# Kernel tuning notes

Measured on AMD Instinct MI355X. Metric: run time of the kernel, lower is better.

## Reference

```python
import jax, jax.numpy as jnp
import numpy as np

DIM = 768
HEADS = 12
HEAD_DIM = DIM // HEADS          # 64
DIM_HALF = HEAD_DIM // 2         # 32
SPATIAL = 3


def _rope_cos_sin(grid, voxel_size, theta):
    """grid: static tuple of ints (len SPATIAL); voxel_size: [SPATIAL] float;
    theta: [H, DIM_HALF] per-head frequency spectrum.
    Returns cos, sin of shape [H, N, DIM_HALF] where N = prod(grid)."""
    axes = [jnp.arange(g, dtype=theta.dtype) for g in grid]
    mesh = jnp.meshgrid(*axes, indexing='ij')
    coords = jnp.stack([m.reshape(-1) for m in mesh], axis=-1) * voxel_size  # [N, S] physical coords
    axis_idx = np.arange(DIM_HALF) % len(grid)        # round-robin freq->axis assignment
    pos = coords[:, axis_idx]                          # [N, DIM_HALF]
    ang = pos[None, :, :] * theta[:, None, :]          # [H, N, DIM_HALF]
    return jnp.cos(ang), jnp.sin(ang)


def _rope_apply(t, cos, sin):
    # t: [B, H, N, D]; cos/sin: [H, N, DIM_HALF] broadcast over batch
    t1, t2 = jnp.split(t, 2, axis=-1)
    return jnp.concatenate([t1 * cos - t2 * sin, t1 * sin + t2 * cos], axis=-1)


def setup_inputs() -> dict:
    key = jax.random.key(0)
    k_x, k_qkv, k_proj, k_b = jax.random.split(key, 4)
    B, N = 2, 8 * 16 * 16
    x = jax.random.normal(k_x, (B, N, DIM), dtype=jnp.float32)
    voxel_size = jnp.ones((SPATIAL,), dtype=jnp.float32)
    # nn.Linear weights are [out_features, in_features]
    w_qkv = jax.random.normal(k_qkv, (3 * DIM, DIM), dtype=jnp.float32) * (DIM ** -0.5)
    w_proj = jax.random.normal(k_proj, (DIM, DIM), dtype=jnp.float32) * (DIM ** -0.5)
    b_proj = jax.random.normal(k_b, (DIM,), dtype=jnp.float32) * 0.02
    # learnable per-head base frequencies: theta_j = 10000^{-j/dim_half}
    base = (1.0 / (10000.0 ** (np.arange(DIM_HALF, dtype=np.float32) / DIM_HALF)))
    theta = jnp.asarray(np.tile(base[None, :], (HEADS, 1)))  # [H, DIM_HALF]
    return {"x": x, "voxel_size": voxel_size, "w_qkv": w_qkv, "w_proj": w_proj,
            "b_proj": b_proj, "theta": theta, "grid_d": 8, "grid_h": 16, "grid_w": 16}


def reference(x, voxel_size, w_qkv, w_proj, b_proj, theta, grid_d, grid_h, grid_w):
    B, N, dim = x.shape
    H, D = HEADS, HEAD_DIM
    qkv = jnp.einsum('bnd,ed->bne', x, w_qkv).reshape(B, N, 3, H, D)
    qkv = jnp.transpose(qkv, (2, 0, 3, 1, 4))           # [3, B, H, N, D]
    q, k, v = qkv[0], qkv[1], qkv[2]
    cos, sin = _rope_cos_sin((grid_d, grid_h, grid_w), voxel_size, theta)
    q = _rope_apply(q, cos, sin)
    k = _rope_apply(k, cos, sin)
    scale = 1.0 / np.sqrt(D).astype(np.float32)
    attn = jax.nn.softmax(jnp.einsum('bhnd,bhmd->bhnm', q, k) * scale, axis=-1)
    out = jnp.einsum('bhnm,bhmd->bhnd', attn, v)        # [B, H, N, D]
    out = jnp.transpose(out, (0, 2, 1, 3)).reshape(B, N, dim)
    return out @ w_proj.T + b_proj
```

## Files before the change

### kernel.cpp

```cpp
#include <hip/hip_runtime.h>
#include <stdint.h>

#define DIM 768
#define NHEADS 12
#define HDIM 64
#define DHALF 32
#define NTOK 2048
#define QKVN 2304
#define LOG2E 1.44269504088896340736f

typedef unsigned short u16;
typedef unsigned int u32;
typedef __bf16 bf16x8 __attribute__((ext_vector_type(8)));
typedef short s16x8 __attribute__((ext_vector_type(8)));
typedef float f32x4 __attribute__((ext_vector_type(4)));

__device__ __forceinline__ f32x4 f4zero() { f32x4 z = {0.f, 0.f, 0.f, 0.f}; return z; }

__device__ __forceinline__ u16 f2bf(float f) {
    u32 u = __builtin_bit_cast(u32, f);
    u32 r = (u + 0x7FFFu + ((u >> 16) & 1u)) >> 16;
    return (u16)r;
}

__device__ __forceinline__ void gld_lds16(void* lds, const void* g) {
    __builtin_amdgcn_global_load_lds((const __attribute__((address_space(1))) u32*)g,
                                     (__attribute__((address_space(3))) u32*)lds,
                                     16, 0, 0);
}

__global__ __launch_bounds__(256) void cast3_f32_to_bf16(const float* __restrict__ a, u16* __restrict__ oa, int na4,
                                                         const float* __restrict__ b, u16* __restrict__ ob, int nb4,
                                                         const float* __restrict__ c, u16* __restrict__ oc, int nc4) {
    int i = blockIdx.x * 256 + threadIdx.x;
    const float* src;
    u16* dst;
    int j = i;
    if (i < na4) { src = a; dst = oa; }
    else if (i < na4 + nb4) { src = b; dst = ob; j = i - na4; }
    else if (i < na4 + nb4 + nc4) { src = c; dst = oc; j = i - na4 - nb4; }
    else return;
    float4 v = ((const float4*)src)[j];
    u32 w0 = (u32)f2bf(v.x) | ((u32)f2bf(v.y) << 16);
    u32 w1 = (u32)f2bf(v.z) | ((u32)f2bf(v.w) << 16);
    ((uint2*)dst)[j] = make_uint2(w0, w1);
}

__global__ __launch_bounds__(256) void gemm_bt(const u16* __restrict__ A, const u16* __restrict__ Bm,
                                               float* __restrict__ C, const float* __restrict__ bias,
                                               int M, int N, int K) {
    __shared__ __align__(16) u16 sA[2][64 * 32];
    __shared__ __align__(16) u16 sB[2][64 * 32];
    const int t = threadIdx.x;
    const int wave = t >> 6, lane = t & 63;
    const int quad = lane >> 4, l16 = lane & 15;
    const int bm = blockIdx.y * 64, bn = blockIdx.x * 64;
    const int wr = wave >> 1, wc = wave & 1;

    f32x4 acc[2][2];
#pragma unroll
    for (int i = 0; i < 2; i++)
#pragma unroll
        for (int j = 0; j < 2; j++) acc[i][j] = f4zero();

    auto stage = [&](int k0, int bi) {
        gld_lds16((char*)&sA[bi][0] + wave * 1024,
                  A + (size_t)(bm + wave * 16 + (lane >> 2)) * K + k0 + (lane & 3) * 8);
        gld_lds16((char*)&sB[bi][0] + wave * 1024,
                  Bm + (size_t)(bn + wave * 16 + (lane >> 2)) * K + k0 + (lane & 3) * 8);
    };

    stage(0, 0);
    int cur = 0;
    for (int k0 = 0; k0 < K; k0 += 32) {
        __syncthreads();
        if (k0 + 32 < K) stage(k0 + 32, cur ^ 1);
        const u16* pA = &sA[cur][0];
        const u16* pB = &sB[cur][0];
        bf16x8 af[2], bfr[2];
#pragma unroll
        for (int mb = 0; mb < 2; mb++)
            af[mb] = *(const bf16x8*)(pA + (wr * 32 + mb * 16 + l16) * 32 + quad * 8);
#pragma unroll
        for (int nb = 0; nb < 2; nb++)
            bfr[nb] = *(const bf16x8*)(pB + (wc * 32 + nb * 16 + l16) * 32 + quad * 8);
#pragma unroll
        for (int mb = 0; mb < 2; mb++)
#pragma unroll
            for (int nb = 0; nb < 2; nb++)
                acc[mb][nb] = __builtin_amdgcn_mfma_f32_16x16x32_bf16(af[mb], bfr[nb], acc[mb][nb], 0, 0, 0);
        cur ^= 1;
    }
#pragma unroll
    for (int mb = 0; mb < 2; mb++)
#pragma unroll
        for (int nb = 0; nb < 2; nb++) {
            int col = bn + wc * 32 + nb * 16 + l16;
            float bv = bias ? bias[col] : 0.f;
#pragma unroll
            for (int r = 0; r < 4; r++) {
                int row = bm + wr * 32 + mb * 16 + quad * 4 + r;
                C[(size_t)row * N + col] = acc[mb][nb][r] + bv;
            }
        }
}

__global__ __launch_bounds__(256) void gemm_qkv_rope(const u16* __restrict__ A, const u16* __restrict__ Bm,
                                                     const float* __restrict__ voxel,
                                                     const float* __restrict__ theta,
                                                     const int* __restrict__ gh_p, const int* __restrict__ gw_p,
                                                     u16* __restrict__ q_s, u16* __restrict__ k_s,
                                                     u16* __restrict__ vT, int M) {
    __shared__ __align__(16) u16 sA[2][128 * 32];
    __shared__ __align__(16) u16 sB[2][64 * 32];
    const int t = threadIdx.x;
    const int wave = t >> 6, lane = t & 63;
    const int quad = lane >> 4, l16 = lane & 15;
    const int bm = blockIdx.y * 128, bn = blockIdx.x * 64;
    const int K = DIM;

    f32x4 acc[2][4];
#pragma unroll
    for (int i = 0; i < 2; i++)
#pragma unroll
        for (int j = 0; j < 4; j++) acc[i][j] = f4zero();

    auto stage = [&](int k0, int bi) {
#pragma unroll
        for (int s = 0; s < 2; ++s) {
            int ci = wave * 2 + s;
            gld_lds16((char*)&sA[bi][0] + ci * 1024,
                      A + (size_t)(bm + ci * 16 + (lane >> 2)) * K + k0 + (lane & 3) * 8);
        }
        gld_lds16((char*)&sB[bi][0] + wave * 1024,
                  Bm + (size_t)(bn + wave * 16 + (lane >> 2)) * K + k0 + (lane & 3) * 8);
    };

    stage(0, 0);
    int cur = 0;
    for (int k0 = 0; k0 < K; k0 += 32) {
        __syncthreads();
        if (k0 + 32 < K) stage(k0 + 32, cur ^ 1);
        const u16* pA = &sA[cur][0];
        const u16* pB = &sB[cur][0];
        bf16x8 af[2], bfr[4];
#pragma unroll
        for (int mb = 0; mb < 2; mb++)
            af[mb] = *(const bf16x8*)(pA + (wave * 32 + mb * 16 + l16) * 32 + quad * 8);
#pragma unroll
        for (int nb = 0; nb < 4; nb++)
            bfr[nb] = *(const bf16x8*)(pB + (nb * 16 + l16) * 32 + quad * 8);
#pragma unroll
        for (int mb = 0; mb < 2; mb++)
#pragma unroll
            for (int nb = 0; nb < 4; nb++)
                acc[mb][nb] = __builtin_amdgcn_mfma_f32_16x16x32_bf16(af[mb], bfr[nb], acc[mb][nb], 0, 0, 0);
        cur ^= 1;
    }

    const int col0 = bn;
    const int typ = col0 / DIM;
    const int h = (col0 % DIM) >> 6;
    const int b = bm / NTOK;
    const int n0 = (bm % NTOK) + wave * 32;
    const size_t bh = (size_t)b * NHEADS + h;

    if (typ == 2) {
        int chunk = ((bm % NTOK) >> 5) + wave;
        u16* base = vT + ((size_t)bh * 64 + chunk) * 2048;
#pragma unroll
        for (int nb = 0; nb < 4; nb++) {
            u32 w0 = (u32)f2bf(acc[0][nb][0]) | ((u32)f2bf(acc[0][nb][1]) << 16);
            u32 w1 = (u32)f2bf(acc[0][nb][2]) | ((u32)f2bf(acc[0][nb][3]) << 16);
            u32 w2 = (u32)f2bf(acc[1][nb][0]) | ((u32)f2bf(acc[1][nb][1]) << 16);
            u32 w3 = (u32)f2bf(acc[1][nb][2]) | ((u32)f2bf(acc[1][nb][3]) << 16);
            *(uint4*)(base + nb * 512 + lane * 8) = make_uint4(w0, w1, w2, w3);
        }
    } else {
        const int gh = *gh_p, gw = *gw_p;
        const bool p2 = ((gw & (gw - 1)) == 0) && ((gh & (gh - 1)) == 0);
        const int wsh = 31 - __builtin_clz(gw), hsh = 31 - __builtin_clz(gh);
        const float qsc = (typ == 0) ? 0.125f * LOG2E : 1.0f;
        const float th0 = theta[h * DHALF + l16];
        const float th1 = theta[h * DHALF + 16 + l16];
        const int ax0 = l16 % 3, ax1 = (16 + l16) % 3;
        const float vx0 = voxel[ax0], vx1 = voxel[ax1];
#pragma unroll
        for (int mb = 0; mb < 2; mb++)
#pragma unroll
            for (int r = 0; r < 4; r++) {
                int n = n0 + mb * 16 + quad * 4 + r;
                int xw, yh, zd;
                if (p2) {
                    xw = n & (gw - 1);
                    int rem = n >> wsh;
                    yh = rem & (gh - 1);
                    zd = rem >> hsh;
                } else {
                    xw = n % gw;
                    int rem = n / gw;
                    yh = rem % gh;
                    zd = rem / gh;
                }
                float c0 = (float)(ax0 == 0 ? zd : (ax0 == 1 ? yh : xw)) * vx0;
                float c1 = (float)(ax1 == 0 ? zd : (ax1 == 1 ? yh : xw)) * vx1;
                float s0, co0, s1, co1;
                __sincosf(c0 * th0, &s0, &co0);
                __sincosf(c1 * th1, &s1, &co1);
                float t1a = acc[mb][0][r], t2a = acc[mb][2][r];
                float o1a = (t1a * co0 - t2a * s0) * qsc, o2a = (t1a * s0 + t2a * co0) * qsc;
                float t1b = acc[mb][1][r], t2b = acc[mb][3][r];
                float o1b = (t1b * co1 - t2b * s1) * qsc, o2b = (t1b * s1 + t2b * co1) * qsc;
                if (typ == 0) {
                    u16* dq = q_s + (bh * NTOK + n) * HDIM;
                    dq[l16] = f2bf(o1a);
                    dq[l16 + DHALF] = f2bf(o2a);
                    dq[16 + l16] = f2bf(o1b);
                    dq[48 + l16] = f2bf(o2b);
                } else {
                    int gm = wave * 2 + mb;
                    int tile_i = ((bm % NTOK) >> 6) + (gm >> 2);
                    int g = gm & 3;
                    int k16 = quad * 4 + r;
                    size_t baseo = bh * (size_t)NTOK * HDIM + (size_t)tile_i * 4096 + g * 1024;
                    int j = l16 & 7;
                    size_t oa = baseo + (size_t)(((l16 >> 3) * 16 + k16) * 8 + j);
                    size_t ob = baseo + (size_t)((((2 + (l16 >> 3)) * 16) + k16) * 8 + j);
                    k_s[oa] = f2bf(o1a);
                    k_s[oa + 512] = f2bf(o2a);
                    k_s[ob] = f2bf(o1b);
                    k_s[ob + 512] = f2bf(o2b);
                }
            }
    }
}

__global__ __launch_bounds__(256) void flash_attn(const u16* __restrict__ Q, const u16* __restrict__ Kp,
                                                  const u16* __restrict__ Vp, u16* __restrict__ Out, int NBH) {
    int i = blockIdx.x;
    int bh_i = i % NBH;
    int qt = i / NBH;
    int b = bh_i / NHEADS, h = bh_i % NHEADS;
    int t = threadIdx.x, wave = t >> 6, lane = t & 63, quad = lane >> 4, l16 = lane & 15;
    size_t bh = (size_t)b * NHEADS + h;
    const u16* Qb = Q + bh * NTOK * HDIM;
    const u16* Kb = Kp + bh * NTOK * HDIM;
    const u16* Vb = Vp + bh * NTOK * HDIM;

    __shared__ __align__(16) u16 smem[2][8192];

    const int q0 = qt * 64 + wave * 16;
    bf16x8 qf[2];
#pragma unroll
    for (int kc = 0; kc < 2; kc++)
        qf[kc] = *(const bf16x8*)(Qb + (size_t)(q0 + l16) * HDIM + kc * 32 + quad * 8);

    s16x8 ov;
#pragma unroll
    for (int j = 0; j < 8; j++) ov[j] = (l16 == 0) ? (short)0x3F80 : (short)0;

    f32x4 o[5];
#pragma unroll
    for (int db = 0; db < 5; db++) o[db] = f4zero();

    auto stage = [&](int kt, int bi) {
        const u16* Kg = Kb + (size_t)kt * 4096;
        const u16* Vg = Vb + (size_t)kt * 4096;
        u16* buf = &smem[bi][0];
#pragma unroll
        for (int s = 0; s < 2; s++) {
            gld_lds16(buf + (wave * 2 + s) * 512, Kg + (wave * 2 + s) * 512 + lane * 8);
            gld_lds16(buf + 4096 + (wave * 2 + s) * 512, Vg + (wave * 2 + s) * 512 + lane * 8);
        }
    };

    stage(0, 0);
    int cur = 0;
    for (int kt = 0; kt < NTOK / 64; ++kt) {
        __syncthreads();
        if (kt + 1 < NTOK / 64) stage(kt + 1, cur ^ 1);
        const u16* sK = &smem[cur][0];
        const u16* sV = &smem[cur][4096];
#pragma unroll
        for (int c = 0; c < 2; ++c) {
            bf16x8 kf[2][2];
#pragma unroll
            for (int kb2 = 0; kb2 < 2; kb2++)
#pragma unroll
                for (int kc = 0; kc < 2; kc++)
                    kf[kb2][kc] = *(const bf16x8*)(sK + ((c * 2 + kb2) * 2 + kc) * 512 + lane * 8);
            s16x8 bv[4];
#pragma unroll
            for (int db = 0; db < 4; db++)
                bv[db] = *(const s16x8*)(sV + c * 2048 + db * 512 + lane * 8);
            f32x4 st0, st1;
            __builtin_amdgcn_s_setprio(1);
            {
                f32x4 z = f4zero();
                z = __builtin_amdgcn_mfma_f32_16x16x32_bf16(kf[0][0], qf[0], z, 0, 0, 0);
                st0 = __builtin_amdgcn_mfma_f32_16x16x32_bf16(kf[0][1], qf[1], z, 0, 0, 0);
                f32x4 z2 = f4zero();
                z2 = __builtin_amdgcn_mfma_f32_16x16x32_bf16(kf[1][0], qf[0], z2, 0, 0, 0);
                st1 = __builtin_amdgcn_mfma_f32_16x16x32_bf16(kf[1][1], qf[1], z2, 0, 0, 0);
            }
            __builtin_amdgcn_s_setprio(0);
            bf16x8 pb;
#pragma unroll
            for (int r = 0; r < 4; r++) {
                pb[r] = (__bf16)__builtin_exp2f(st0[r]);
                pb[r + 4] = (__bf16)__builtin_exp2f(st1[r]);
            }
            __builtin_amdgcn_s_setprio(1);
#pragma unroll
            for (int db = 0; db < 4; db++)
                o[db] = __builtin_amdgcn_mfma_f32_16x16x32_bf16(pb, __builtin_bit_cast(bf16x8, bv[db]),
                                                                o[db], 0, 0, 0);
            o[4] = __builtin_amdgcn_mfma_f32_16x16x32_bf16(pb, __builtin_bit_cast(bf16x8, ov),
                                                           o[4], 0, 0, 0);
            __builtin_amdgcn_s_setprio(0);
        }
        cur ^= 1;
    }

#pragma unroll
    for (int r = 0; r < 4; r++) {
        float s = __shfl(o[4][r], lane & 48);
        float inv = 1.0f / s;
        int n = q0 + quad * 4 + r;
        u16* dst = Out + ((size_t)b * NTOK + n) * DIM + h * HDIM + l16;
#pragma unroll
        for (int db = 0; db < 4; db++)
            dst[db * 16] = f2bf(o[db][r] * inv);
    }
}

extern "C" void kernel_launch(void* const* d_in, const int* in_sizes, int n_in,
                              void* d_out, int out_size, void* d_ws, size_t ws_size,
                              hipStream_t stream) {
    const float* x = (const float*)d_in[0];
    const float* voxel = (const float*)d_in[1];
    const float* w_qkv = (const float*)d_in[2];
    const float* w_proj = (const float*)d_in[3];
    const float* b_proj = (const float*)d_in[4];
    const float* theta = (const float*)d_in[5];
    const int* gh_p = (const int*)d_in[7];
    const int* gw_p = (const int*)d_in[8];
    const int B = in_sizes[0] / (NTOK * DIM);
    const int M = B * NTOK;

    char* p = (char*)d_ws;
    u16* xb = (u16*)p;       p += (size_t)M * DIM * 2;
    u16* wqkvb = (u16*)p;    p += (size_t)3 * DIM * DIM * 2;
    u16* wprojb = (u16*)p;   p += (size_t)DIM * DIM * 2;
    u16* q_s = (u16*)p;      p += (size_t)M * DIM * 2;
    u16* k_s = (u16*)p;      p += (size_t)M * DIM * 2;
    u16* vT = (u16*)p;       p += (size_t)M * DIM * 2;
    u16* attn = (u16*)p;     p += (size_t)M * DIM * 2;

    int na4 = M * DIM / 4, nb4 = 3 * DIM * DIM / 4, nc4 = DIM * DIM / 4;
    cast3_f32_to_bf16<<<dim3((na4 + nb4 + nc4 + 255) / 256), 256, 0, stream>>>(
        x, xb, na4, w_qkv, wqkvb, nb4, w_proj, wprojb, nc4);

    gemm_qkv_rope<<<dim3(QKVN / 64, M / 128), 256, 0, stream>>>(
        xb, wqkvb, voxel, theta, gh_p, gw_p, q_s, k_s, vT, M);

    flash_attn<<<dim3((B * NHEADS * NTOK) / 64), 256, 0, stream>>>(q_s, k_s, vT, attn, B * NHEADS);

    gemm_bt<<<dim3(DIM / 64, M / 64), 256, 0, stream>>>(attn, wprojb, (float*)d_out, b_proj, M, DIM, DIM);
}
```

Measured before the change: 174.5 us.

## Split KV across wave pairs and reuse K/V fragments across two query tiles

Each wave now owns 32 query rows (two 16-row tiles) instead of 16. The four waves are split into two groups, each handling half of the key sequence, so K/V fragments read from LDS are reused for both query tiles. The two partial accumulators (including the row-sum column) are combined through a new LDS exchange buffer before normalization and store. This roughly halves LDS fragment reads per MFMA, at the cost of more accumulator registers, about 20KB of extra shared memory that may lower occupancy, and an extra barrier with a reduction step at the end.

```diff
diff --git a/kernel.cpp b/kernel.cpp
--- a/kernel.cpp
+++ b/kernel.cpp
@@ -242,66 +242,71 @@
     int qt = i / NBH;
     int b = bh_i / NHEADS, h = bh_i % NHEADS;
     int t = threadIdx.x, wave = t >> 6, lane = t & 63, quad = lane >> 4, l16 = lane & 15;
+    const int qs = wave & 1;
+    const int ks = wave >> 1;
     size_t bh = (size_t)b * NHEADS + h;
     const u16* Qb = Q + bh * NTOK * HDIM;
     const u16* Kb = Kp + bh * NTOK * HDIM;
     const u16* Vb = Vp + bh * NTOK * HDIM;
 
     __shared__ __align__(16) u16 smem[2][8192];
-
-    const int q0 = qt * 64 + wave * 16;
-    bf16x8 qf[2];
-#pragma unroll
-    for (int kc = 0; kc < 2; kc++)
-        qf[kc] = *(const bf16x8*)(Qb + (size_t)(q0 + l16) * HDIM + kc * 32 + quad * 8);
+    __shared__ f32x4 xch[128][10];
+
+    const int q0 = qt * 64 + qs * 32;
+    bf16x8 qf[2][2];
+#pragma unroll
+    for (int qb = 0; qb < 2; qb++)
+#pragma unroll
+        for (int kc = 0; kc < 2; kc++)
+            qf[qb][kc] = *(const bf16x8*)(Qb + (size_t)(q0 + qb * 16 + l16) * HDIM + kc * 32 + quad * 8);
 
     s16x8 ov;
 #pragma unroll
     for (int j = 0; j < 8; j++) ov[j] = (l16 == 0) ? (short)0x3F80 : (short)0;
 
-    f32x4 o[5];
-#pragma unroll
-    for (int db = 0; db < 5; db++) o[db] = f4zero();
-
-    auto stage = [&](int kt, int bi) {
-        const u16* Kg = Kb + (size_t)kt * 4096;
-        const u16* Vg = Vb + (size_t)kt * 4096;
-        u16* buf = &smem[bi][0];
-#pragma unroll
-        for (int s = 0; s < 2; s++) {
-            gld_lds16(buf + (wave * 2 + s) * 512, Kg + (wave * 2 + s) * 512 + lane * 8);
-            gld_lds16(buf + 4096 + (wave * 2 + s) * 512, Vg + (wave * 2 + s) * 512 + lane * 8);
-        }
+    f32x4 o[2][5];
+#pragma unroll
+    for (int qb = 0; qb < 2; qb++)
+#pragma unroll
+        for (int db = 0; db < 5; db++) o[qb][db] = f4zero();
+
+    auto stage = [&](int j, int bi) {
+        const u16* src = (wave & 1) ? Vb : Kb;
+        int chunk = j + (wave >> 1) * 32;
+        u16* dst = &smem[bi][wave * 2048];
+#pragma unroll
+        for (int s = 0; s < 4; s++)
+            gld_lds16(dst + s * 512, src + (size_t)chunk * 2048 + s * 512 + lane * 8);
     };
 
     stage(0, 0);
     int cur = 0;
-    for (int kt = 0; kt < NTOK / 64; ++kt) {
+    for (int j = 0; j < 32; ++j) {
         __syncthreads();
-        if (kt + 1 < NTOK / 64) stage(kt + 1, cur ^ 1);
-        const u16* sK = &smem[cur][0];
-        const u16* sV = &smem[cur][4096];
-#pragma unroll
-        for (int c = 0; c < 2; ++c) {
-            bf16x8 kf[2][2];
-#pragma unroll
-            for (int kb2 = 0; kb2 < 2; kb2++)
-#pragma unroll
-                for (int kc = 0; kc < 2; kc++)
-                    kf[kb2][kc] = *(const bf16x8*)(sK + ((c * 2 + kb2) * 2 + kc) * 512 + lane * 8);
-            s16x8 bv[4];
-#pragma unroll
-            for (int db = 0; db < 4; db++)
-                bv[db] = *(const s16x8*)(sV + c * 2048 + db * 512 + lane * 8);
+        if (j + 1 < 32) stage(j + 1, cur ^ 1);
+        const u16* sK = &smem[cur][ks * 4096];
+        const u16* sV = sK + 2048;
+        bf16x8 kf[2][2];
+#pragma unroll
+        for (int kb2 = 0; kb2 < 2; kb2++)
+#pragma unroll
+            for (int kc = 0; kc < 2; kc++)
+                kf[kb2][kc] = *(const bf16x8*)(sK + (kb2 * 2 + kc) * 512 + lane * 8);
+        s16x8 bv[4];
+#pragma unroll
+        for (int db = 0; db < 4; db++)
+            bv[db] = *(const s16x8*)(sV + db * 512 + lane * 8);
+#pragma unroll
+        for (int qb = 0; qb < 2; qb++) {
             f32x4 st0, st1;
             __builtin_amdgcn_s_setprio(1);
             {
                 f32x4 z = f4zero();
-                z = __builtin_amdgcn_mfma_f32_16x16x32_bf16(kf[0][0], qf[0], z, 0, 0, 0);
-                st0 = __builtin_amdgcn_mfma_f32_16x16x32_bf16(kf[0][1], qf[1], z, 0, 0, 0);
+                z = __builtin_amdgcn_mfma_f32_16x16x32_bf16(kf[0][0], qf[qb][0], z, 0, 0, 0);
+                st0 = __builtin_amdgcn_mfma_f32_16x16x32_bf16(kf[0][1], qf[qb][1], z, 0, 0, 0);
                 f32x4 z2 = f4zero();
-                z2 = __builtin_amdgcn_mfma_f32_16x16x32_bf16(kf[1][0], qf[0], z2, 0, 0, 0);
-                st1 = __builtin_amdgcn_mfma_f32_16x16x32_bf16(kf[1][1], qf[1], z2, 0, 0, 0);
+                z2 = __builtin_amdgcn_mfma_f32_16x16x32_bf16(kf[1][0], qf[qb][0], z2, 0, 0, 0);
+                st1 = __builtin_amdgcn_mfma_f32_16x16x32_bf16(kf[1][1], qf[qb][1], z2, 0, 0, 0);
             }
             __builtin_amdgcn_s_setprio(0);
             bf16x8 pb;
@@ -313,24 +318,41 @@
             __builtin_amdgcn_s_setprio(1);
 #pragma unroll
             for (int db = 0; db < 4; db++)
-                o[db] = __builtin_amdgcn_mfma_f32_16x16x32_bf16(pb, __builtin_bit_cast(bf16x8, bv[db]),
-                                                                o[db], 0, 0, 0);
-            o[4] = __builtin_amdgcn_mfma_f32_16x16x32_bf16(pb, __builtin_bit_cast(bf16x8, ov),
-                                                           o[4], 0, 0, 0);
+                o[qb][db] = __builtin_amdgcn_mfma_f32_16x16x32_bf16(pb, __builtin_bit_cast(bf16x8, bv[db]),
+                                                                   o[qb][db], 0, 0, 0);
+            o[qb][4] = __builtin_amdgcn_mfma_f32_16x16x32_bf16(pb, __builtin_bit_cast(bf16x8, ov),
+                                                               o[qb][4], 0, 0, 0);
             __builtin_amdgcn_s_setprio(0);
         }
         cur ^= 1;
     }
 
-#pragma unroll
-    for (int r = 0; r < 4; r++) {
-        float s = __shfl(o[4][r], lane & 48);
-        float inv = 1.0f / s;
-        int n = q0 + quad * 4 + r;
-        u16* dst = Out + ((size_t)b * NTOK + n) * DIM + h * HDIM + l16;
-#pragma unroll
-        for (int db = 0; db < 4; db++)
-            dst[db * 16] = f2bf(o[db][r] * inv);
+    const int slot = qs * 64 + lane;
+    if (ks == 1) {
+#pragma unroll
+        for (int qb = 0; qb < 2; qb++)
+#pragma unroll
+            for (int db = 0; db < 5; db++)
+                xch[slot][qb * 5 + db] = o[qb][db];
+    }
+    __syncthreads();
+    if (ks == 0) {
+#pragma unroll
+        for (int qb = 0; qb < 2; qb++) {
+#pragma unroll
+            for (int db = 0; db < 5; db++)
+                o[qb][db] += xch[slot][qb * 5 + db];
+#pragma unroll
+            for (int r = 0; r < 4; r++) {
+                float s = __shfl(o[qb][4][r], lane & 48);
+                float inv = 1.0f / s;
+                int n = q0 + qb * 16 + quad * 4 + r;
+                u16* dst = Out + ((size_t)b * NTOK + n) * DIM + h * HDIM + l16;
+#pragma unroll
+                for (int db = 0; db < 4; db++)
+                    dst[db * 16] = f2bf(o[qb][db][r] * inv);
+            }
+        }
     }
 }
 
```

After: 182.0 us. +4.3%, slower.
